# Kernel optimization log

Measured on AMD Instinct MI355X. Metric: run time of the kernel, lower is better.

The kernel has to match this reference:

```python
import jax, jax.numpy as jnp
import numpy as np
from jax import lax

EPS = 1e-8

def _conv(x, w, b):
    # x: [B,Cin,H,W], w: [Cout,Cin,kh,kw] (torch OIHW layout), SAME padding, stride 1
    y = lax.conv_general_dilated(x, w, (1, 1), 'SAME',
                                 dimension_numbers=('NCHW', 'OIHW', 'NCHW'))
    return y + b[None, :, None, None]

def setup_inputs() -> dict:
    key = jax.random.key(0)
    ks = jax.random.split(key, 16)
    B, S, H, A, NZ, NO = 256, 4, 32, 5, 150, 17
    d = {
        'map_in': jax.random.uniform(ks[0], (B, 2, H, H), jnp.float32),
        'b0': jax.random.uniform(ks[1], (B, H, H), jnp.float32),
        'act_in': jax.random.randint(ks[2], (B, S), 0, A),
        'obs_in': jax.random.uniform(ks[3], (B, S, 4), jnp.float32),
        'is_start': 1,
        'step_size': S,
        'VI_k': 64,
        # parameters, initialized per the torch init scheme
        'Tb_w': 1.0 / 9.0 + jax.random.normal(ks[4], (A, 1, 3, 3)) / 90.0,
        'Tb_b': jnp.zeros((A,)),
        'Tv_w': 1.0 / 9.0 + jax.random.normal(ks[5], (A, 1, 3, 3)) / 90.0,
        'Tv_b': jnp.zeros((A,)),
        'Z1_w': jax.random.normal(ks[6], (NZ, 1, 3, 3)) / 3.0,
        'Z1_b': jnp.zeros((NZ,)),
        'Z2_w': jax.random.normal(ks[7], (NO, NZ, 1, 1)) / np.sqrt(NZ),
        'Z2_b': jnp.zeros((NO,)),
        'O1_w': jax.random.normal(ks[8], (NO, 4)) * 0.25,
        'O1_b': jnp.zeros((NO,)),
        'O3_w': jax.random.normal(ks[9], (NO, NO)) / NO,
        'O3_b': jnp.zeros((NO,)),
        'R1_w': jax.random.normal(ks[10], (NZ, 2, 3, 3)) / np.sqrt(18.0),
        'R1_b': jnp.zeros((NZ,)),
        'R2_w': jax.random.normal(ks[11], (A, NZ, 1, 1)) / np.sqrt(NZ),
        'R2_b': jnp.zeros((A,)),
        'FL_w': jax.random.normal(ks[12], (A, A)) * 0.25,
        'FL_b': jnp.zeros((A,)),
    }
    return d

def reference(map_in, b0, act_in, obs_in, is_start, step_size, VI_k,
              Tb_w, Tb_b, Tv_w, Tv_b, Z1_w, Z1_b, Z2_w, Z2_b,
              O1_w, O1_b, O3_w, O3_b, R1_w, R1_b, R2_w, R2_b, FL_w, FL_b):
    B, _, H, W = map_in.shape
    A = Tb_w.shape[0]

    # ---- VI: value iteration conv+add+max loop ----
    R = _conv(jax.nn.relu(_conv(map_in, R1_w, R1_b)), R2_w, R2_b)  # [B,A,H,W]
    v0 = jnp.zeros((B, 1, H, W), map_in.dtype)
    Q0 = jnp.zeros_like(R)

    def vi_step(carry, _):
        v, _Q = carry
        Q = _conv(v, Tv_w, Tv_b) + R
        v = jnp.max(Q, axis=1, keepdims=True)
        return (v, Q), None

    (_, Q), _ = lax.scan(vi_step, (v0, Q0), None, length=VI_k)
    Q = jnp.transpose(Q, (0, 2, 3, 1))  # [B,H,W,A]

    # ---- observation model Z ----
    Z = jax.nn.sigmoid(_conv(_conv(map_in[:, :1], Z1_w, Z1_b), Z2_w, Z2_b))
    Z = jnp.transpose(Z, (0, 2, 3, 1))  # [B,H,W,17]
    Z = Z / (jnp.sum(Z, axis=3, keepdims=True) + EPS)

    # ---- recurrent Bayes filter + policy ----
    b = b0 if is_start else b0  # is_start resets belief to b0 (always true here)
    outs = []
    for t in range(step_size):  # small fixed recurrence length
        o = obs_in[:, t]  # [B,4]
        w = jax.nn.softmax(jnp.tanh(o @ O1_w.T + O1_b) @ O3_w.T + O3_b, axis=1)  # [B,17]
        Z_O = jnp.einsum('bhwo,bo->bhw', Z, w)
        bp = jnp.transpose(_conv(b[:, None], Tb_w, Tb_b), (0, 2, 3, 1))  # [B,H,W,A]
        a1h = jax.nn.one_hot(act_in[:, t], A, dtype=bp.dtype)
        b_pa = jnp.einsum('bhwa,ba->bhw', bp, a1h)
        b_next = b_pa * Z_O
        b = b_next / (jnp.sum(b_next, axis=(1, 2), keepdims=True) + EPS)
        Qb = jnp.einsum('bhwa,bhw->ba', Q, b)
        outs.append(Qb @ FL_w.T + FL_b)
    outputs = jnp.concatenate(outs, axis=0)  # [step_size*B, A]
    return outputs, b
```

## Files before the change

### kernel.cpp

```cpp
#include <hip/hip_runtime.h>

#define EPSV 1e-8f
#define PW   34
#define NPIX 1024
#define NA   5
#define NOUT 17
#define NZC  150
#define MAXS 8

__global__ __launch_bounds__(1024, 4) void vin_fused(
    const float* __restrict__ map_in, const float* __restrict__ b0,
    const int*   __restrict__ act_in, const float* __restrict__ obs_in,
    const int*   __restrict__ step_p, const int*   __restrict__ vik_p,
    const float* __restrict__ Tb_w,  const float* __restrict__ Tb_b,
    const float* __restrict__ Tv_w,  const float* __restrict__ Tv_b,
    const float* __restrict__ Z1_w,  const float* __restrict__ Z1_b,
    const float* __restrict__ Z2_w,  const float* __restrict__ Z2_b,
    const float* __restrict__ O1_w,  const float* __restrict__ O1_b,
    const float* __restrict__ O3_w,  const float* __restrict__ O3_b,
    const float* __restrict__ R1_w,  const float* __restrict__ R1_b,
    const float* __restrict__ R2_w,  const float* __restrict__ R2_b,
    const float* __restrict__ FL_w,  const float* __restrict__ FL_b,
    float* __restrict__ out, int B)
{
    __shared__ float map0[PW*PW], map1[PW*PW], v_lds[PW*PW], b_lds[PW*PW];
    __shared__ float zc_w[NOUT*9], zc_b[NOUT];
    __shared__ float h_all[MAXS][NOUT], u_all[MAXS][NOUT], w_all[MAXS][NOUT];
    __shared__ float zo_lds[MAXS * NPIX];
    __shared__ float partials[16][6], sums[6];

    const int tid  = threadIdx.x;
    const int blk  = blockIdx.x;
    const int y    = tid >> 5, x = tid & 31;
    const int pidx = (y + 1) * PW + (x + 1);
    const int lane = tid & 63, wvid = tid >> 6;

    const int S = step_p[0];
    const int K = vik_p[0];

    for (int i = tid; i < PW*PW; i += NPIX) {
        map0[i] = 0.f; map1[i] = 0.f; v_lds[i] = 0.f; b_lds[i] = 0.f;
    }
    __syncthreads();
    map0[pidx]  = map_in[blk*2*NPIX + tid];
    map1[pidx]  = map_in[blk*2*NPIX + NPIX + tid];
    b_lds[pidx] = b0[blk*NPIX + tid];

    if (tid < NOUT*9) {
        const int o = tid / 9, k = tid % 9;
        float s = 0.f;
        for (int c = 0; c < NZC; ++c) s += Z2_w[o*NZC + c] * Z1_w[c*9 + k];
        zc_w[tid] = s;
    } else if (tid < NOUT*9 + NOUT) {
        const int o = tid - NOUT*9;
        float s = Z2_b[o];
        for (int c = 0; c < NZC; ++c) s += Z2_w[o*NZC + c] * Z1_b[c];
        zc_b[o] = s;
    }

    const int mt = tid - 256;
    const int mT = mt / NOUT, mO = mt % NOUT;
    if (mt >= 0 && mt < S*NOUT) {
        const float* ob = obs_in + (blk*S + mT)*4;
        float hh = O1_b[mO];
        #pragma unroll
        for (int k = 0; k < 4; ++k) hh += ob[k] * O1_w[mO*4 + k];
        h_all[mT][mO] = tanhf(hh);
    }
    __syncthreads();
    if (mt >= 0 && mt < S*NOUT) {
        float u = O3_b[mO];
        #pragma unroll
        for (int j = 0; j < NOUT; ++j) u += h_all[mT][j] * O3_w[mO*NOUT + j];
        u_all[mT][mO] = u;
    }
    __syncthreads();
    if (mt >= 0 && mt < S*NOUT) {
        float mx = u_all[mT][0];
        #pragma unroll
        for (int j = 1; j < NOUT; ++j) mx = fmaxf(mx, u_all[mT][j]);
        float sm = 0.f;
        #pragma unroll
        for (int j = 0; j < NOUT; ++j) sm += expf(u_all[mT][j] - mx);
        w_all[mT][mO] = expf(u_all[mT][mO] - mx) / sm;
    }
    __syncthreads();

    float m0[9], m1[9];
    #pragma unroll
    for (int k = 0; k < 9; ++k) {
        const int off = (y + k/3)*PW + x + (k%3);
        m0[k] = map0[off]; m1[k] = map1[off];
    }

    float rA[NA], rB[NA];
    #pragma unroll
    for (int a = 0; a < NA; ++a) { rA[a] = R2_b[a]; rB[a] = 0.f; }
    for (int c = 0; c < NZC; c += 2) {
        const float* w1a = R1_w + c*18;
        const float* w1b = w1a + 18;
        float s0 = R1_b[c], s1 = R1_b[c+1];
        #pragma unroll
        for (int k = 0; k < 9; ++k) { s0 += m0[k] * w1a[k];   s1 += m0[k] * w1b[k]; }
        #pragma unroll
        for (int k = 0; k < 9; ++k) { s0 += m1[k] * w1a[9+k]; s1 += m1[k] * w1b[9+k]; }
        s0 = fmaxf(s0, 0.f); s1 = fmaxf(s1, 0.f);
        #pragma unroll
        for (int a = 0; a < NA; ++a) {
            rA[a] += R2_w[a*NZC + c]     * s0;
            rB[a] += R2_w[a*NZC + c + 1] * s1;
        }
    }
    float r[NA];
    #pragma unroll
    for (int a = 0; a < NA; ++a) r[a] = rA[a] + rB[a];

    {
        float z[NOUT];
        float zs = 0.f;
        #pragma unroll
        for (int o = 0; o < NOUT; ++o) {
            float s = zc_b[o];
            #pragma unroll
            for (int k = 0; k < 9; ++k) s += m0[k] * zc_w[o*9 + k];
            const float zz = 1.f / (1.f + expf(-s));
            z[o] = zz; zs += zz;
        }
        const float zn = 1.f / (zs + EPSV);
        for (int t = 0; t < S; ++t) {
            float zo = 0.f;
            #pragma unroll
            for (int o = 0; o < NOUT; ++o) zo += z[o] * w_all[t][o];
            zo_lds[t*NPIX + tid] = zo * zn;
        }
    }

    float q[NA];
    #pragma unroll
    for (int a = 0; a < NA; ++a) q[a] = 0.f;
    for (int it = 0; it < K; ++it) {
        float n[9];
        #pragma unroll
        for (int k = 0; k < 9; ++k) n[k] = v_lds[(y + k/3)*PW + x + (k%3)];
        float vmax = -3.4e38f;
        #pragma unroll
        for (int a = 0; a < NA; ++a) {
            float s = Tv_b[a] + r[a];
            #pragma unroll
            for (int k = 0; k < 9; ++k) s += n[k] * Tv_w[a*9 + k];
            q[a] = s;
            vmax = fmaxf(vmax, s);
        }
        __syncthreads();
        v_lds[pidx] = vmax;
        __syncthreads();
    }

    for (int t = 0; t < S; ++t) {
        const int a_t = act_in[blk*S + t];
        float bp = Tb_b[a_t];
        #pragma unroll
        for (int k = 0; k < 9; ++k)
            bp += b_lds[(y + k/3)*PW + x + (k%3)] * Tb_w[a_t*9 + k];

        const float bn = bp * zo_lds[t*NPIX + tid];

        float v6[6];
        v6[5] = bn;
        #pragma unroll
        for (int a = 0; a < NA; ++a) v6[a] = q[a] * bn;
        #pragma unroll
        for (int k = 0; k < 6; ++k) {
            float vv = v6[k];
            for (int off = 32; off > 0; off >>= 1) vv += __shfl_down(vv, off);
            v6[k] = vv;
        }
        if (lane == 0) {
            #pragma unroll
            for (int k = 0; k < 6; ++k) partials[wvid][k] = v6[k];
        }
        __syncthreads();
        if (tid < 6) {
            float s = 0.f;
            for (int w2 = 0; w2 < 16; ++w2) s += partials[w2][tid];
            sums[tid] = s;
        }
        __syncthreads();

        const float inv = 1.f / (sums[5] + EPSV);
        if (tid < NA) {
            float oj = FL_b[tid];
            #pragma unroll
            for (int a = 0; a < NA; ++a) oj += (sums[a] * inv) * FL_w[tid*NA + a];
            out[(t*B + blk)*NA + tid] = oj;
        }
        b_lds[pidx] = bn * inv;
        __syncthreads();
    }

    out[S*B*NA + blk*NPIX + tid] = b_lds[pidx];
}

extern "C" void kernel_launch(void* const* d_in, const int* in_sizes, int n_in,
                              void* d_out, int out_size, void* d_ws, size_t ws_size,
                              hipStream_t stream)
{
    const float* map_in = (const float*)d_in[0];
    const float* b0     = (const float*)d_in[1];
    const int*   act_in = (const int*)  d_in[2];
    const float* obs_in = (const float*)d_in[3];
    const int*   step_p = (const int*)  d_in[5];
    const int*   vik_p  = (const int*)  d_in[6];
    const float* Tb_w = (const float*)d_in[7];
    const float* Tb_b = (const float*)d_in[8];
    const float* Tv_w = (const float*)d_in[9];
    const float* Tv_b = (const float*)d_in[10];
    const float* Z1_w = (const float*)d_in[11];
    const float* Z1_b = (const float*)d_in[12];
    const float* Z2_w = (const float*)d_in[13];
    const float* Z2_b = (const float*)d_in[14];
    const float* O1_w = (const float*)d_in[15];
    const float* O1_b = (const float*)d_in[16];
    const float* O3_w = (const float*)d_in[17];
    const float* O3_b = (const float*)d_in[18];
    const float* R1_w = (const float*)d_in[19];
    const float* R1_b = (const float*)d_in[20];
    const float* R2_w = (const float*)d_in[21];
    const float* R2_b = (const float*)d_in[22];
    const float* FL_w = (const float*)d_in[23];
    const float* FL_b = (const float*)d_in[24];

    const int B = in_sizes[1] / NPIX;

    hipLaunchKernelGGL(vin_fused, dim3(B), dim3(1024), 0, stream,
        map_in, b0, act_in, obs_in, step_p, vik_p,
        Tb_w, Tb_b, Tv_w, Tv_b, Z1_w, Z1_b, Z2_w, Z2_b,
        O1_w, O1_b, O3_w, O3_b, R1_w, R1_b, R2_w, R2_b,
        FL_w, FL_b, (float*)d_out, B);
}
```

Measured before the change: 187.6 us.

## Split fused kernel into prep, reward/observation, and VI/filter kernels

Breaks the single 1024-thread fused kernel into three launches. The first computes the softmax observation weights and the folded Z conv weights. The second computes the reward map and the normalized observation likelihoods in 256-thread strip blocks. The third runs value iteration and the Bayes filter, reading those intermediates from workspace. The aim is to cut LDS use and register pressure in the long VI loop and to spread the heavy R1/R2 convolution over more, smaller blocks, at the cost of extra launches and global round-trips for r and zo.

```diff
diff --git a/kernel.cpp b/kernel.cpp
--- a/kernel.cpp
+++ b/kernel.cpp
@@ -8,25 +8,141 @@
 #define NZC  150
 #define MAXS 8
 
-__global__ __launch_bounds__(1024, 4) void vin_fused(
-    const float* __restrict__ map_in, const float* __restrict__ b0,
-    const int*   __restrict__ act_in, const float* __restrict__ obs_in,
-    const int*   __restrict__ step_p, const int*   __restrict__ vik_p,
-    const float* __restrict__ Tb_w,  const float* __restrict__ Tb_b,
-    const float* __restrict__ Tv_w,  const float* __restrict__ Tv_b,
-    const float* __restrict__ Z1_w,  const float* __restrict__ Z1_b,
-    const float* __restrict__ Z2_w,  const float* __restrict__ Z2_b,
-    const float* __restrict__ O1_w,  const float* __restrict__ O1_b,
-    const float* __restrict__ O3_w,  const float* __restrict__ O3_b,
-    const float* __restrict__ R1_w,  const float* __restrict__ R1_b,
-    const float* __restrict__ R2_w,  const float* __restrict__ R2_b,
-    const float* __restrict__ FL_w,  const float* __restrict__ FL_b,
+__global__ __launch_bounds__(256) void k0_prep(
+    const float* __restrict__ obs_in,
+    const float* __restrict__ O1_w, const float* __restrict__ O1_b,
+    const float* __restrict__ O3_w, const float* __restrict__ O3_b,
+    const float* __restrict__ Z1_w, const float* __restrict__ Z1_b,
+    const float* __restrict__ Z2_w, const float* __restrict__ Z2_b,
+    float* __restrict__ w_all, float* __restrict__ zc, int S)
+{
+    __shared__ float h[MAXS*NOUT], u[MAXS*NOUT];
+    const int tid = threadIdx.x, b = blockIdx.x;
+    const int t = tid / NOUT, o = tid % NOUT;
+    const bool act = (tid < S*NOUT);
+
+    if (act) {
+        const float* ob = obs_in + (b*S + t)*4;
+        float hh = O1_b[o];
+        #pragma unroll
+        for (int k = 0; k < 4; ++k) hh += ob[k] * O1_w[o*4 + k];
+        h[tid] = tanhf(hh);
+    }
+    __syncthreads();
+    if (act) {
+        float uu = O3_b[o];
+        #pragma unroll
+        for (int j = 0; j < NOUT; ++j) uu += h[t*NOUT + j] * O3_w[o*NOUT + j];
+        u[tid] = uu;
+    }
+    __syncthreads();
+    if (act) {
+        float mx = u[t*NOUT];
+        #pragma unroll
+        for (int j = 1; j < NOUT; ++j) mx = fmaxf(mx, u[t*NOUT + j]);
+        float sm = 0.f;
+        #pragma unroll
+        for (int j = 0; j < NOUT; ++j) sm += expf(u[t*NOUT + j] - mx);
+        w_all[(b*MAXS + t)*NOUT + o] = expf(u[tid] - mx) / sm;
+    }
+    if (b == 0) {
+        for (int j2 = tid; j2 < NOUT*9 + NOUT; j2 += 256) {
+            if (j2 < NOUT*9) {
+                const int oo = j2 / 9, k = j2 % 9;
+                float s = 0.f;
+                for (int c = 0; c < NZC; ++c) s += Z2_w[oo*NZC + c] * Z1_w[c*9 + k];
+                zc[j2] = s;
+            } else {
+                const int oo = j2 - NOUT*9;
+                float s = Z2_b[oo];
+                for (int c = 0; c < NZC; ++c) s += Z2_w[oo*NZC + c] * Z1_b[c];
+                zc[j2] = s;
+            }
+        }
+    }
+}
+
+__global__ __launch_bounds__(256, 4) void k1_rz(
+    const float* __restrict__ map_in,
+    const float* __restrict__ R1_w, const float* __restrict__ R1_b,
+    const float* __restrict__ R2_w, const float* __restrict__ R2_b,
+    const float* __restrict__ w_all, const float* __restrict__ zc,
+    float* __restrict__ r_out, float* __restrict__ zo_out, int S)
+{
+    __shared__ float t0[10*34], t1[10*34];
+    const int tid = threadIdx.x;
+    const int b = blockIdx.x >> 2, strip = blockIdx.x & 3;
+    const int ty = tid >> 5, x = tid & 31;
+    const int y = strip*8 + ty;
+    const int pix = y*32 + x;
+
+    for (int i = tid; i < 340; i += 256) {
+        const int tr = i / 34, tc = i % 34;
+        const int gy = strip*8 - 1 + tr, gx = tc - 1;
+        const bool ok = (gy >= 0 && gy < 32 && gx >= 0 && gx < 32);
+        t0[i] = ok ? map_in[b*2*NPIX + gy*32 + gx] : 0.f;
+        t1[i] = ok ? map_in[b*2*NPIX + NPIX + gy*32 + gx] : 0.f;
+    }
+    __syncthreads();
+
+    float m0[9], m1[9];
+    #pragma unroll
+    for (int k = 0; k < 9; ++k) {
+        const int off = (ty + k/3)*34 + x + (k%3);
+        m0[k] = t0[off]; m1[k] = t1[off];
+    }
+
+    float rA[NA], rB[NA];
+    #pragma unroll
+    for (int a = 0; a < NA; ++a) { rA[a] = R2_b[a]; rB[a] = 0.f; }
+    for (int c = 0; c < NZC; c += 2) {
+        const float* w1a = R1_w + c*18;
+        const float* w1b = w1a + 18;
+        float s0 = R1_b[c], s1 = R1_b[c+1];
+        #pragma unroll
+        for (int k = 0; k < 9; ++k) { s0 += m0[k] * w1a[k];   s1 += m0[k] * w1b[k]; }
+        #pragma unroll
+        for (int k = 0; k < 9; ++k) { s0 += m1[k] * w1a[9+k]; s1 += m1[k] * w1b[9+k]; }
+        s0 = fmaxf(s0, 0.f); s1 = fmaxf(s1, 0.f);
+        #pragma unroll
+        for (int a = 0; a < NA; ++a) {
+            rA[a] += R2_w[a*NZC + c]     * s0;
+            rB[a] += R2_w[a*NZC + c + 1] * s1;
+        }
+    }
+    #pragma unroll
+    for (int a = 0; a < NA; ++a)
+        r_out[(b*NA + a)*NPIX + pix] = rA[a] + rB[a];
+
+    float z[NOUT];
+    float zs = 0.f;
+    #pragma unroll
+    for (int o = 0; o < NOUT; ++o) {
+        float s = zc[NOUT*9 + o];
+        #pragma unroll
+        for (int k = 0; k < 9; ++k) s += m0[k] * zc[o*9 + k];
+        const float zz = 1.f / (1.f + expf(-s));
+        z[o] = zz; zs += zz;
+    }
+    const float zn = 1.f / (zs + EPSV);
+    for (int t = 0; t < S; ++t) {
+        float zo = 0.f;
+        #pragma unroll
+        for (int o = 0; o < NOUT; ++o) zo += z[o] * w_all[(b*MAXS + t)*NOUT + o];
+        zo_out[(b*S + t)*NPIX + pix] = zo * zn;
+    }
+}
+
+__global__ __launch_bounds__(1024, 4) void k2_vib(
+    const float* __restrict__ b0,   const int* __restrict__ act_in,
+    const int*   __restrict__ step_p, const int* __restrict__ vik_p,
+    const float* __restrict__ Tb_w, const float* __restrict__ Tb_b,
+    const float* __restrict__ Tv_w, const float* __restrict__ Tv_b,
+    const float* __restrict__ FL_w, const float* __restrict__ FL_b,
+    const float* __restrict__ r_in, const float* __restrict__ zo_in,
     float* __restrict__ out, int B)
 {
-    __shared__ float map0[PW*PW], map1[PW*PW], v_lds[PW*PW], b_lds[PW*PW];
-    __shared__ float zc_w[NOUT*9], zc_b[NOUT];
-    __shared__ float h_all[MAXS][NOUT], u_all[MAXS][NOUT], w_all[MAXS][NOUT];
-    __shared__ float zo_lds[MAXS * NPIX];
+    __shared__ float v_lds[PW*PW], b_lds[PW*PW];
     __shared__ float partials[16][6], sums[6];
 
     const int tid  = threadIdx.x;
@@ -38,102 +154,14 @@
     const int S = step_p[0];
     const int K = vik_p[0];
 
-    for (int i = tid; i < PW*PW; i += NPIX) {
-        map0[i] = 0.f; map1[i] = 0.f; v_lds[i] = 0.f; b_lds[i] = 0.f;
-    }
-    __syncthreads();
-    map0[pidx]  = map_in[blk*2*NPIX + tid];
-    map1[pidx]  = map_in[blk*2*NPIX + NPIX + tid];
+    for (int i = tid; i < PW*PW; i += NPIX) { v_lds[i] = 0.f; b_lds[i] = 0.f; }
+    __syncthreads();
     b_lds[pidx] = b0[blk*NPIX + tid];
 
-    if (tid < NOUT*9) {
-        const int o = tid / 9, k = tid % 9;
-        float s = 0.f;
-        for (int c = 0; c < NZC; ++c) s += Z2_w[o*NZC + c] * Z1_w[c*9 + k];
-        zc_w[tid] = s;
-    } else if (tid < NOUT*9 + NOUT) {
-        const int o = tid - NOUT*9;
-        float s = Z2_b[o];
-        for (int c = 0; c < NZC; ++c) s += Z2_w[o*NZC + c] * Z1_b[c];
-        zc_b[o] = s;
-    }
-
-    const int mt = tid - 256;
-    const int mT = mt / NOUT, mO = mt % NOUT;
-    if (mt >= 0 && mt < S*NOUT) {
-        const float* ob = obs_in + (blk*S + mT)*4;
-        float hh = O1_b[mO];
-        #pragma unroll
-        for (int k = 0; k < 4; ++k) hh += ob[k] * O1_w[mO*4 + k];
-        h_all[mT][mO] = tanhf(hh);
-    }
-    __syncthreads();
-    if (mt >= 0 && mt < S*NOUT) {
-        float u = O3_b[mO];
-        #pragma unroll
-        for (int j = 0; j < NOUT; ++j) u += h_all[mT][j] * O3_w[mO*NOUT + j];
-        u_all[mT][mO] = u;
-    }
-    __syncthreads();
-    if (mt >= 0 && mt < S*NOUT) {
-        float mx = u_all[mT][0];
-        #pragma unroll
-        for (int j = 1; j < NOUT; ++j) mx = fmaxf(mx, u_all[mT][j]);
-        float sm = 0.f;
-        #pragma unroll
-        for (int j = 0; j < NOUT; ++j) sm += expf(u_all[mT][j] - mx);
-        w_all[mT][mO] = expf(u_all[mT][mO] - mx) / sm;
-    }
-    __syncthreads();
-
-    float m0[9], m1[9];
-    #pragma unroll
-    for (int k = 0; k < 9; ++k) {
-        const int off = (y + k/3)*PW + x + (k%3);
-        m0[k] = map0[off]; m1[k] = map1[off];
-    }
-
-    float rA[NA], rB[NA];
-    #pragma unroll
-    for (int a = 0; a < NA; ++a) { rA[a] = R2_b[a]; rB[a] = 0.f; }
-    for (int c = 0; c < NZC; c += 2) {
-        const float* w1a = R1_w + c*18;
-        const float* w1b = w1a + 18;
-        float s0 = R1_b[c], s1 = R1_b[c+1];
-        #pragma unroll
-        for (int k = 0; k < 9; ++k) { s0 += m0[k] * w1a[k];   s1 += m0[k] * w1b[k]; }
-        #pragma unroll
-        for (int k = 0; k < 9; ++k) { s0 += m1[k] * w1a[9+k]; s1 += m1[k] * w1b[9+k]; }
-        s0 = fmaxf(s0, 0.f); s1 = fmaxf(s1, 0.f);
-        #pragma unroll
-        for (int a = 0; a < NA; ++a) {
-            rA[a] += R2_w[a*NZC + c]     * s0;
-            rB[a] += R2_w[a*NZC + c + 1] * s1;
-        }
-    }
     float r[NA];
     #pragma unroll
-    for (int a = 0; a < NA; ++a) r[a] = rA[a] + rB[a];
-
-    {
-        float z[NOUT];
-        float zs = 0.f;
-        #pragma unroll
-        for (int o = 0; o < NOUT; ++o) {
-            float s = zc_b[o];
-            #pragma unroll
-            for (int k = 0; k < 9; ++k) s += m0[k] * zc_w[o*9 + k];
-            const float zz = 1.f / (1.f + expf(-s));
-            z[o] = zz; zs += zz;
-        }
-        const float zn = 1.f / (zs + EPSV);
-        for (int t = 0; t < S; ++t) {
-            float zo = 0.f;
-            #pragma unroll
-            for (int o = 0; o < NOUT; ++o) zo += z[o] * w_all[t][o];
-            zo_lds[t*NPIX + tid] = zo * zn;
-        }
-    }
+    for (int a = 0; a < NA; ++a)
+        r[a] = r_in[(blk*NA + a)*NPIX + tid] + Tv_b[a];
 
     float q[NA];
     #pragma unroll
@@ -145,7 +173,7 @@
         float vmax = -3.4e38f;
         #pragma unroll
         for (int a = 0; a < NA; ++a) {
-            float s = Tv_b[a] + r[a];
+            float s = r[a];
             #pragma unroll
             for (int k = 0; k < 9; ++k) s += n[k] * Tv_w[a*9 + k];
             q[a] = s;
@@ -163,7 +191,7 @@
         for (int k = 0; k < 9; ++k)
             bp += b_lds[(y + k/3)*PW + x + (k%3)] * Tb_w[a_t*9 + k];
 
-        const float bn = bp * zo_lds[t*NPIX + tid];
+        const float bn = bp * zo_in[(blk*S + t)*NPIX + tid];
 
         float v6[6];
         v6[5] = bn;
@@ -231,10 +259,21 @@
     const float* FL_b = (const float*)d_in[24];
 
     const int B = in_sizes[1] / NPIX;
-
-    hipLaunchKernelGGL(vin_fused, dim3(B), dim3(1024), 0, stream,
-        map_in, b0, act_in, obs_in, step_p, vik_p,
-        Tb_w, Tb_b, Tv_w, Tv_b, Z1_w, Z1_b, Z2_w, Z2_b,
-        O1_w, O1_b, O3_w, O3_b, R1_w, R1_b, R2_w, R2_b,
-        FL_w, FL_b, (float*)d_out, B);
-}
+    const int S = in_sizes[2] / B;
+
+    float* ws    = (float*)d_ws;
+    float* w_all = ws;
+    float* zc    = w_all + (size_t)B*MAXS*NOUT;
+    float* r_ws  = zc + 192;
+    float* zo_ws = r_ws + (size_t)B*NA*NPIX;
+
+    hipLaunchKernelGGL(k0_prep, dim3(B), dim3(256), 0, stream,
+        obs_in, O1_w, O1_b, O3_w, O3_b, Z1_w, Z1_b, Z2_w, Z2_b, w_all, zc, S);
+
+    hipLaunchKernelGGL(k1_rz, dim3(B*4), dim3(256), 0, stream,
+        map_in, R1_w, R1_b, R2_w, R2_b, w_all, zc, r_ws, zo_ws, S);
+
+    hipLaunchKernelGGL(k2_vib, dim3(B), dim3(1024), 0, stream,
+        b0, act_in, step_p, vik_p, Tb_w, Tb_b, Tv_w, Tv_b, FL_w, FL_b,
+        r_ws, zo_ws, (float*)d_out, B);
+}
```

New measurement: 214.1 us. 1.14x slower.
